# Performance work log

Hardware: AMD Instinct MI355X
Metric: run time of the kernel (lower is better)

The kernel has to match this reference:

```python
import jax, jax.numpy as jnp
import numpy as np

NUM_NODES = 100000
EMBED_DIM = 128
NUM_RELATIONS = 64
BATCH = 512


def setup_inputs() -> dict:
    key = jax.random.key(0)
    k1, k2, k3, k4, k5 = jax.random.split(key, 5)
    u = jax.random.randint(k1, (BATCH,), 0, NUM_NODES)
    v = jax.random.randint(k2, (BATCH,), 0, NUM_NODES)
    r = jax.random.randint(k3, (BATCH,), 0, NUM_RELATIONS)
    node_embeddings = jax.random.normal(k4, (NUM_NODES, EMBED_DIM), dtype=jnp.float32)
    relation_matrices = jax.random.normal(k5, (NUM_RELATIONS, EMBED_DIM, EMBED_DIM), dtype=jnp.float32)
    return {"u": u, "v": v, "r": r,
            "node_embeddings": node_embeddings,
            "relation_matrices": relation_matrices}


def reference(u, v, r, node_embeddings, relation_matrices):
    u_embed = node_embeddings[u]            # [B, D]
    v_embed = node_embeddings[v]            # [B, D]
    rel = relation_matrices[r]              # [B, D, D] per-sample gathered matrices
    # torch.matmul([B,D], [B,D,D]) broadcasts u_embed over the relation batch -> [B_rel, B_u, D]
    score = jnp.einsum('ud,bde->bue', u_embed, rel)   # [B, B, D]
    # matmul with v_embed.T [D, B] -> [B, B, B]
    score = jnp.einsum('bue,ve->buv', score, v_embed)  # [B, B, B]
    return jax.nn.sigmoid(score)
```

## Files before the change

kernel.cpp:

```cpp
#include <hip/hip_runtime.h>


#define BATCH 512
#define DIM   128
#define NRELS 64
#define NTHR  256

typedef float floatx4 __attribute__((ext_vector_type(4)));

__global__ __launch_bounds__(NTHR, 4)
void rad_phaseA_kernel(const int* __restrict__ u_idx,
                       const float* __restrict__ nodes,
                       const float* __restrict__ rels,
                       float* __restrict__ T_ws)
{
    const int rel = (int)blockIdx.x >> 3;
    const int ut0 = ((int)blockIdx.x & 7) * 64;

    __shared__ __align__(16) float UEsT[DIM * 64];
    __shared__ __align__(16) float Rs[16 * DIM];

    const int t  = (int)threadIdx.x;
    const int tu = t >> 4;
    const int tx = t & 15;

    for (int i = t; i < 64 * (DIM / 4); i += NTHR) {
        const int row = i & 63;
        const int dc  = i >> 6;
        const float4 val = *reinterpret_cast<const float4*>(
            nodes + (size_t)u_idx[ut0 + row] * DIM + dc * 4);
        UEsT[(dc * 4 + 0) * 64 + row] = val.x;
        UEsT[(dc * 4 + 1) * 64 + row] = val.y;
        UEsT[(dc * 4 + 2) * 64 + row] = val.z;
        UEsT[(dc * 4 + 3) * 64 + row] = val.w;
    }

    float accA[4][8];
    #pragma unroll
    for (int i = 0; i < 4; ++i)
        #pragma unroll
        for (int j = 0; j < 8; ++j) accA[i][j] = 0.f;

    const float* Rbase = rels + (size_t)rel * DIM * DIM;
    for (int dch = 0; dch < DIM / 16; ++dch) {
        __syncthreads();
        for (int i = t; i < 16 * (DIM / 4); i += NTHR) {
            const int rr = i >> 5;
            const int cc = i & 31;
            *reinterpret_cast<float4*>(Rs + rr * DIM + cc * 4) =
                *reinterpret_cast<const float4*>(
                    Rbase + (size_t)(dch * 16 + rr) * DIM + cc * 4);
        }
        __syncthreads();
        #pragma unroll
        for (int dd = 0; dd < 16; ++dd) {
            const int d = dch * 16 + dd;
            const float4 a  = *reinterpret_cast<const float4*>(UEsT + d * 64 + tu * 4);
            const float4 b0 = *reinterpret_cast<const float4*>(Rs + dd * DIM + tx * 4);
            const float4 b1 = *reinterpret_cast<const float4*>(Rs + dd * DIM + 64 + tx * 4);
            const float av[4] = {a.x, a.y, a.z, a.w};
            const float bv[8] = {b0.x, b0.y, b0.z, b0.w, b1.x, b1.y, b1.z, b1.w};
            #pragma unroll
            for (int i = 0; i < 4; ++i)
                #pragma unroll
                for (int j = 0; j < 8; ++j)
                    accA[i][j] = fmaf(av[i], bv[j], accA[i][j]);
        }
    }

    #pragma unroll
    for (int i = 0; i < 4; ++i) {
        float* rowp = T_ws + ((size_t)rel * BATCH + ut0 + tu * 4 + i) * DIM;
        *reinterpret_cast<float4*>(rowp + tx * 4) =
            make_float4(accA[i][0], accA[i][1], accA[i][2], accA[i][3]);
        *reinterpret_cast<float4*>(rowp + 64 + tx * 4) =
            make_float4(accA[i][4], accA[i][5], accA[i][6], accA[i][7]);
    }
}

__global__ __launch_bounds__(NTHR, 2)
void rad_phaseB_kernel(const int* __restrict__ v_idx,
                       const int* __restrict__ r_idx,
                       const float* __restrict__ nodes,
                       const float* __restrict__ T_ws,
                       float* __restrict__ out)
{
    const int bid = (int)blockIdx.x;
    const int rel = bid >> 6;
    const int ut0 = ((bid >> 3) & 7) * 64;
    const int vt0 = (bid & 7) * 64;

    __shared__ int s_match[BATCH];
    __shared__ int s_mc;
    __shared__ __align__(16) float TsT[DIM * 64];
    __shared__ __align__(16) float VEsT[DIM * 64];

    const int t  = (int)threadIdx.x;
    const int tu = t >> 4;
    const int tx = t & 15;

    if (t == 0) s_mc = 0;
    __syncthreads();
    for (int i = t; i < BATCH; i += NTHR) {
        if (r_idx[i] == rel) {
            int p = atomicAdd(&s_mc, 1);
            s_match[p] = i;
        }
    }
    __syncthreads();
    const int mc = s_mc;
    if (mc == 0) return;

    for (int i = t; i < 64 * (DIM / 4); i += NTHR) {
        const int row = i & 63;
        const int ec  = i >> 6;
        const float4 val = *reinterpret_cast<const float4*>(
            T_ws + ((size_t)rel * BATCH + ut0 + row) * DIM + ec * 4);
        TsT[(ec * 4 + 0) * 64 + row] = val.x;
        TsT[(ec * 4 + 1) * 64 + row] = val.y;
        TsT[(ec * 4 + 2) * 64 + row] = val.z;
        TsT[(ec * 4 + 3) * 64 + row] = val.w;
    }
    for (int i = t; i < 64 * (DIM / 4); i += NTHR) {
        const int row = i & 63;
        const int ec  = i >> 6;
        const float4 val = *reinterpret_cast<const float4*>(
            nodes + (size_t)v_idx[vt0 + row] * DIM + ec * 4);
        VEsT[(ec * 4 + 0) * 64 + row] = val.x;
        VEsT[(ec * 4 + 1) * 64 + row] = val.y;
        VEsT[(ec * 4 + 2) * 64 + row] = val.z;
        VEsT[(ec * 4 + 3) * 64 + row] = val.w;
    }
    __syncthreads();

    float acc[4][4];
    #pragma unroll
    for (int i = 0; i < 4; ++i)
        #pragma unroll
        for (int j = 0; j < 4; ++j) acc[i][j] = 0.f;

    #pragma unroll 8
    for (int e = 0; e < DIM; ++e) {
        const float4 a = *reinterpret_cast<const float4*>(TsT  + e * 64 + tu * 4);
        const float4 b = *reinterpret_cast<const float4*>(VEsT + e * 64 + tx * 4);
        const float av[4] = {a.x, a.y, a.z, a.w};
        const float bv[4] = {b.x, b.y, b.z, b.w};
        #pragma unroll
        for (int i = 0; i < 4; ++i)
            #pragma unroll
            for (int j = 0; j < 4; ++j)
                acc[i][j] = fmaf(av[i], bv[j], acc[i][j]);
    }

    floatx4 sg[4];
    #pragma unroll
    for (int i = 0; i < 4; ++i) {
        sg[i].x = 1.f / (1.f + __expf(-acc[i][0]));
        sg[i].y = 1.f / (1.f + __expf(-acc[i][1]));
        sg[i].z = 1.f / (1.f + __expf(-acc[i][2]));
        sg[i].w = 1.f / (1.f + __expf(-acc[i][3]));
    }

    for (int m = 0; m < mc; ++m) {
        const int bb = s_match[m];
        float* obase = out + (size_t)bb * BATCH * BATCH;
        #pragma unroll
        for (int i = 0; i < 4; ++i) {
            floatx4* dst = reinterpret_cast<floatx4*>(
                obase + (size_t)(ut0 + tu * 4 + i) * BATCH + vt0 + tx * 4);
            __builtin_nontemporal_store(sg[i], dst);
        }
    }
}

__global__ __launch_bounds__(NTHR, 2)
void rad_fused_kernel(const int* __restrict__ u_idx,
                      const int* __restrict__ v_idx,
                      const int* __restrict__ r_idx,
                      const float* __restrict__ nodes,
                      const float* __restrict__ rels,
                      float* __restrict__ out)
{
    const int rel = (int)blockIdx.x >> 3;
    const int ut0 = ((int)blockIdx.x & 7) * 64;

    __shared__ int s_match[BATCH];
    __shared__ int s_mc;
    __shared__ __align__(16) float s_TsT[DIM * 64];
    __shared__ __align__(16) float s_buf[DIM * 64 + 16 * DIM];

    const int t  = (int)threadIdx.x;
    const int tu = t >> 4;
    const int tx = t & 15;

    if (t == 0) s_mc = 0;
    __syncthreads();
    for (int i = t; i < BATCH; i += NTHR) {
        if (r_idx[i] == rel) {
            int p = atomicAdd(&s_mc, 1);
            s_match[p] = i;
        }
    }

    float* UEsT = s_buf;
    float* Rs   = s_buf + DIM * 64;

    for (int i = t; i < 64 * (DIM / 4); i += NTHR) {
        const int row = i & 63;
        const int dc  = i >> 6;
        const float4 val = *reinterpret_cast<const float4*>(
            nodes + (size_t)u_idx[ut0 + row] * DIM + dc * 4);
        UEsT[(dc * 4 + 0) * 64 + row] = val.x;
        UEsT[(dc * 4 + 1) * 64 + row] = val.y;
        UEsT[(dc * 4 + 2) * 64 + row] = val.z;
        UEsT[(dc * 4 + 3) * 64 + row] = val.w;
    }
    __syncthreads();
    const int mc = s_mc;
    if (mc == 0) return;

    float accA[4][8];
    #pragma unroll
    for (int i = 0; i < 4; ++i)
        #pragma unroll
        for (int j = 0; j < 8; ++j) accA[i][j] = 0.f;

    const float* Rbase = rels + (size_t)rel * DIM * DIM;
    for (int dch = 0; dch < DIM / 16; ++dch) {
        for (int i = t; i < 16 * (DIM / 4); i += NTHR) {
            const int rr = i >> 5;
            const int cc = i & 31;
            *reinterpret_cast<float4*>(Rs + rr * DIM + cc * 4) =
                *reinterpret_cast<const float4*>(
                    Rbase + (size_t)(dch * 16 + rr) * DIM + cc * 4);
        }
        __syncthreads();
        #pragma unroll
        for (int dd = 0; dd < 16; ++dd) {
            const int d = dch * 16 + dd;
            const float4 a  = *reinterpret_cast<const float4*>(UEsT + d * 64 + tu * 4);
            const float4 b0 = *reinterpret_cast<const float4*>(Rs + dd * DIM + tx * 4);
            const float4 b1 = *reinterpret_cast<const float4*>(Rs + dd * DIM + 64 + tx * 4);
            const float av[4] = {a.x, a.y, a.z, a.w};
            const float bv[8] = {b0.x, b0.y, b0.z, b0.w, b1.x, b1.y, b1.z, b1.w};
            #pragma unroll
            for (int i = 0; i < 4; ++i)
                #pragma unroll
                for (int j = 0; j < 8; ++j)
                    accA[i][j] = fmaf(av[i], bv[j], accA[i][j]);
        }
        __syncthreads();
    }

    #pragma unroll
    for (int j = 0; j < 8; ++j) {
        const int e = (j < 4) ? (tx * 4 + j) : (64 + tx * 4 + (j - 4));
        #pragma unroll
        for (int i = 0; i < 4; ++i)
            s_TsT[e * 64 + tu * 4 + i] = accA[i][j];
    }

    float* VEsT = s_buf;
    for (int vt = 0; vt < BATCH / 64; ++vt) {
        __syncthreads();
        for (int i = t; i < 64 * (DIM / 4); i += NTHR) {
            const int row = i & 63;
            const int ec  = i >> 6;
            const float4 val = *reinterpret_cast<const float4*>(
                nodes + (size_t)v_idx[vt * 64 + row] * DIM + ec * 4);
            VEsT[(ec * 4 + 0) * 64 + row] = val.x;
            VEsT[(ec * 4 + 1) * 64 + row] = val.y;
            VEsT[(ec * 4 + 2) * 64 + row] = val.z;
            VEsT[(ec * 4 + 3) * 64 + row] = val.w;
        }
        __syncthreads();

        float acc[4][4];
        #pragma unroll
        for (int i = 0; i < 4; ++i)
            #pragma unroll
            for (int j = 0; j < 4; ++j) acc[i][j] = 0.f;

        #pragma unroll 8
        for (int e = 0; e < DIM; ++e) {
            const float4 a = *reinterpret_cast<const float4*>(s_TsT + e * 64 + tu * 4);
            const float4 b = *reinterpret_cast<const float4*>(VEsT  + e * 64 + tx * 4);
            const float av[4] = {a.x, a.y, a.z, a.w};
            const float bv[4] = {b.x, b.y, b.z, b.w};
            #pragma unroll
            for (int i = 0; i < 4; ++i)
                #pragma unroll
                for (int j = 0; j < 4; ++j)
                    acc[i][j] = fmaf(av[i], bv[j], acc[i][j]);
        }

        floatx4 sg[4];
        #pragma unroll
        for (int i = 0; i < 4; ++i) {
            sg[i].x = 1.f / (1.f + __expf(-acc[i][0]));
            sg[i].y = 1.f / (1.f + __expf(-acc[i][1]));
            sg[i].z = 1.f / (1.f + __expf(-acc[i][2]));
            sg[i].w = 1.f / (1.f + __expf(-acc[i][3]));
        }

        for (int m = 0; m < mc; ++m) {
            const int bb = s_match[m];
            float* obase = out + (size_t)bb * BATCH * BATCH;
            #pragma unroll
            for (int i = 0; i < 4; ++i) {
                floatx4* dst = reinterpret_cast<floatx4*>(
                    obase + (size_t)(ut0 + tu * 4 + i) * BATCH + vt * 64 + tx * 4);
                __builtin_nontemporal_store(sg[i], dst);
            }
        }
    }
}

extern "C" void kernel_launch(void* const* d_in, const int* in_sizes, int n_in,
                              void* d_out, int out_size, void* d_ws, size_t ws_size,
                              hipStream_t stream) {
    const int*   u_idx = (const int*)d_in[0];
    const int*   v_idx = (const int*)d_in[1];
    const int*   r_idx = (const int*)d_in[2];
    const float* nodes = (const float*)d_in[3];
    const float* rels  = (const float*)d_in[4];
    float* out = (float*)d_out;

    const size_t t_bytes = (size_t)NRELS * BATCH * DIM * sizeof(float);
    if (ws_size >= t_bytes) {
        float* T_ws = (float*)d_ws;
        rad_phaseA_kernel<<<dim3(NRELS * 8), dim3(NTHR), 0, stream>>>(
            u_idx, nodes, rels, T_ws);
        rad_phaseB_kernel<<<dim3(NRELS * 8 * 8), dim3(NTHR), 0, stream>>>(
            v_idx, r_idx, nodes, T_ws, out);
    } else {
        rad_fused_kernel<<<dim3(NRELS * 8), dim3(NTHR), 0, stream>>>(
            u_idx, v_idx, r_idx, nodes, rels, out);
    }
}
```

Before: 157.3 us.

## Materialize per-relation score planes then broadcast-copy into output

Replaces the two-phase scheme, which wrote a T workspace and then did per-tile scattered stores to every matching batch row, with a new pipeline. The first kernel computes the full sigmoid score plane S for each of the 64 relations in a single fused kernel. The second kernel is a plain streaming copy from S[r[b]] into out[b]. The aim is to make the 512 MB output write a uniform, load-balanced stream and avoid the uneven per-block work in the old phase B. In exchange it adds a 64 MB intermediate write and a full read of S during the copy, and it needs a larger workspace or else it falls back to the fused kernel.

```diff
diff --git a/kernel.cpp b/kernel.cpp
--- a/kernel.cpp
+++ b/kernel.cpp
@@ -8,21 +8,25 @@
 
 typedef float floatx4 __attribute__((ext_vector_type(4)));
 
-__global__ __launch_bounds__(NTHR, 4)
-void rad_phaseA_kernel(const int* __restrict__ u_idx,
-                       const float* __restrict__ nodes,
-                       const float* __restrict__ rels,
-                       float* __restrict__ T_ws)
+__global__ __launch_bounds__(NTHR, 2)
+void rad_computeS_kernel(const int* __restrict__ u_idx,
+                         const int* __restrict__ v_idx,
+                         const float* __restrict__ nodes,
+                         const float* __restrict__ rels,
+                         float* __restrict__ S)
 {
     const int rel = (int)blockIdx.x >> 3;
     const int ut0 = ((int)blockIdx.x & 7) * 64;
 
-    __shared__ __align__(16) float UEsT[DIM * 64];
-    __shared__ __align__(16) float Rs[16 * DIM];
+    __shared__ __align__(16) float s_TsT[DIM * 64];
+    __shared__ __align__(16) float s_buf[DIM * 64 + 16 * DIM];
 
     const int t  = (int)threadIdx.x;
     const int tu = t >> 4;
     const int tx = t & 15;
+
+    float* UEsT = s_buf;
+    float* Rs   = s_buf + DIM * 64;
 
     for (int i = t; i < 64 * (DIM / 4); i += NTHR) {
         const int row = i & 63;
@@ -34,6 +38,7 @@
         UEsT[(dc * 4 + 2) * 64 + row] = val.z;
         UEsT[(dc * 4 + 3) * 64 + row] = val.w;
     }
+    __syncthreads();
 
     float accA[4][8];
     #pragma unroll
@@ -43,7 +48,6 @@
 
     const float* Rbase = rels + (size_t)rel * DIM * DIM;
     for (int dch = 0; dch < DIM / 16; ++dch) {
-        __syncthreads();
         for (int i = t; i < 16 * (DIM / 4); i += NTHR) {
             const int rr = i >> 5;
             const int cc = i & 31;
@@ -66,110 +70,84 @@
                 for (int j = 0; j < 8; ++j)
                     accA[i][j] = fmaf(av[i], bv[j], accA[i][j]);
         }
+        __syncthreads();
     }
 
     #pragma unroll
-    for (int i = 0; i < 4; ++i) {
-        float* rowp = T_ws + ((size_t)rel * BATCH + ut0 + tu * 4 + i) * DIM;
-        *reinterpret_cast<float4*>(rowp + tx * 4) =
-            make_float4(accA[i][0], accA[i][1], accA[i][2], accA[i][3]);
-        *reinterpret_cast<float4*>(rowp + 64 + tx * 4) =
-            make_float4(accA[i][4], accA[i][5], accA[i][6], accA[i][7]);
+    for (int j = 0; j < 8; ++j) {
+        const int e = (j < 4) ? (tx * 4 + j) : (64 + tx * 4 + (j - 4));
+        #pragma unroll
+        for (int i = 0; i < 4; ++i)
+            s_TsT[e * 64 + tu * 4 + i] = accA[i][j];
+    }
+
+    float* VEsT = s_buf;
+    float* Splane = S + (size_t)rel * BATCH * BATCH;
+    for (int vt = 0; vt < BATCH / 64; ++vt) {
+        __syncthreads();
+        for (int i = t; i < 64 * (DIM / 4); i += NTHR) {
+            const int row = i & 63;
+            const int ec  = i >> 6;
+            const float4 val = *reinterpret_cast<const float4*>(
+                nodes + (size_t)v_idx[vt * 64 + row] * DIM + ec * 4);
+            VEsT[(ec * 4 + 0) * 64 + row] = val.x;
+            VEsT[(ec * 4 + 1) * 64 + row] = val.y;
+            VEsT[(ec * 4 + 2) * 64 + row] = val.z;
+            VEsT[(ec * 4 + 3) * 64 + row] = val.w;
+        }
+        __syncthreads();
+
+        float acc[4][4];
+        #pragma unroll
+        for (int i = 0; i < 4; ++i)
+            #pragma unroll
+            for (int j = 0; j < 4; ++j) acc[i][j] = 0.f;
+
+        #pragma unroll 8
+        for (int e = 0; e < DIM; ++e) {
+            const float4 a = *reinterpret_cast<const float4*>(s_TsT + e * 64 + tu * 4);
+            const float4 b = *reinterpret_cast<const float4*>(VEsT  + e * 64 + tx * 4);
+            const float av[4] = {a.x, a.y, a.z, a.w};
+            const float bv[4] = {b.x, b.y, b.z, b.w};
+            #pragma unroll
+            for (int i = 0; i < 4; ++i)
+                #pragma unroll
+                for (int j = 0; j < 4; ++j)
+                    acc[i][j] = fmaf(av[i], bv[j], acc[i][j]);
+        }
+
+        #pragma unroll
+        for (int i = 0; i < 4; ++i) {
+            float4 sg;
+            sg.x = 1.f / (1.f + __expf(-acc[i][0]));
+            sg.y = 1.f / (1.f + __expf(-acc[i][1]));
+            sg.z = 1.f / (1.f + __expf(-acc[i][2]));
+            sg.w = 1.f / (1.f + __expf(-acc[i][3]));
+            *reinterpret_cast<float4*>(
+                Splane + (size_t)(ut0 + tu * 4 + i) * BATCH + vt * 64 + tx * 4) = sg;
+        }
     }
 }
 
-__global__ __launch_bounds__(NTHR, 2)
-void rad_phaseB_kernel(const int* __restrict__ v_idx,
-                       const int* __restrict__ r_idx,
-                       const float* __restrict__ nodes,
-                       const float* __restrict__ T_ws,
-                       float* __restrict__ out)
+__global__ __launch_bounds__(NTHR)
+void rad_copy_kernel(const int* __restrict__ r_idx,
+                     const float* __restrict__ S,
+                     float* __restrict__ out)
 {
-    const int bid = (int)blockIdx.x;
-    const int rel = bid >> 6;
-    const int ut0 = ((bid >> 3) & 7) * 64;
-    const int vt0 = (bid & 7) * 64;
-
-    __shared__ int s_match[BATCH];
-    __shared__ int s_mc;
-    __shared__ __align__(16) float TsT[DIM * 64];
-    __shared__ __align__(16) float VEsT[DIM * 64];
-
-    const int t  = (int)threadIdx.x;
-    const int tu = t >> 4;
-    const int tx = t & 15;
-
-    if (t == 0) s_mc = 0;
-    __syncthreads();
-    for (int i = t; i < BATCH; i += NTHR) {
-        if (r_idx[i] == rel) {
-            int p = atomicAdd(&s_mc, 1);
-            s_match[p] = i;
-        }
-    }
-    __syncthreads();
-    const int mc = s_mc;
-    if (mc == 0) return;
-
-    for (int i = t; i < 64 * (DIM / 4); i += NTHR) {
-        const int row = i & 63;
-        const int ec  = i >> 6;
-        const float4 val = *reinterpret_cast<const float4*>(
-            T_ws + ((size_t)rel * BATCH + ut0 + row) * DIM + ec * 4);
-        TsT[(ec * 4 + 0) * 64 + row] = val.x;
-        TsT[(ec * 4 + 1) * 64 + row] = val.y;
-        TsT[(ec * 4 + 2) * 64 + row] = val.z;
-        TsT[(ec * 4 + 3) * 64 + row] = val.w;
-    }
-    for (int i = t; i < 64 * (DIM / 4); i += NTHR) {
-        const int row = i & 63;
-        const int ec  = i >> 6;
-        const float4 val = *reinterpret_cast<const float4*>(
-            nodes + (size_t)v_idx[vt0 + row] * DIM + ec * 4);
-        VEsT[(ec * 4 + 0) * 64 + row] = val.x;
-        VEsT[(ec * 4 + 1) * 64 + row] = val.y;
-        VEsT[(ec * 4 + 2) * 64 + row] = val.z;
-        VEsT[(ec * 4 + 3) * 64 + row] = val.w;
-    }
-    __syncthreads();
-
-    float acc[4][4];
-    #pragma unroll
-    for (int i = 0; i < 4; ++i)
-        #pragma unroll
-        for (int j = 0; j < 4; ++j) acc[i][j] = 0.f;
-
-    #pragma unroll 8
-    for (int e = 0; e < DIM; ++e) {
-        const float4 a = *reinterpret_cast<const float4*>(TsT  + e * 64 + tu * 4);
-        const float4 b = *reinterpret_cast<const float4*>(VEsT + e * 64 + tx * 4);
-        const float av[4] = {a.x, a.y, a.z, a.w};
-        const float bv[4] = {b.x, b.y, b.z, b.w};
-        #pragma unroll
-        for (int i = 0; i < 4; ++i)
-            #pragma unroll
-            for (int j = 0; j < 4; ++j)
-                acc[i][j] = fmaf(av[i], bv[j], acc[i][j]);
-    }
-
-    floatx4 sg[4];
-    #pragma unroll
-    for (int i = 0; i < 4; ++i) {
-        sg[i].x = 1.f / (1.f + __expf(-acc[i][0]));
-        sg[i].y = 1.f / (1.f + __expf(-acc[i][1]));
-        sg[i].z = 1.f / (1.f + __expf(-acc[i][2]));
-        sg[i].w = 1.f / (1.f + __expf(-acc[i][3]));
-    }
-
-    for (int m = 0; m < mc; ++m) {
-        const int bb = s_match[m];
-        float* obase = out + (size_t)bb * BATCH * BATCH;
-        #pragma unroll
-        for (int i = 0; i < 4; ++i) {
-            floatx4* dst = reinterpret_cast<floatx4*>(
-                obase + (size_t)(ut0 + tu * 4 + i) * BATCH + vt0 + tx * 4);
-            __builtin_nontemporal_store(sg[i], dst);
-        }
+    const int bid   = (int)blockIdx.x;
+    const int b     = bid >> 3;
+    const int slice = bid & 7;
+    const int rel   = r_idx[b];
+
+    const float* src = S   + ((size_t)rel * BATCH + slice * 64) * BATCH;
+    float*       dst = out + ((size_t)b   * BATCH + slice * 64) * BATCH;
+
+    const int t = (int)threadIdx.x;
+    #pragma unroll 4
+    for (int i = t; i < 64 * BATCH / 4; i += NTHR) {
+        const floatx4 v = *reinterpret_cast<const floatx4*>(src + i * 4);
+        __builtin_nontemporal_store(
+            v, reinterpret_cast<floatx4*>(dst + i * 4));
     }
 }
 
@@ -326,13 +304,13 @@
     const float* rels  = (const float*)d_in[4];
     float* out = (float*)d_out;
 
-    const size_t t_bytes = (size_t)NRELS * BATCH * DIM * sizeof(float);
-    if (ws_size >= t_bytes) {
-        float* T_ws = (float*)d_ws;
-        rad_phaseA_kernel<<<dim3(NRELS * 8), dim3(NTHR), 0, stream>>>(
-            u_idx, nodes, rels, T_ws);
-        rad_phaseB_kernel<<<dim3(NRELS * 8 * 8), dim3(NTHR), 0, stream>>>(
-            v_idx, r_idx, nodes, T_ws, out);
+    const size_t s_bytes = (size_t)NRELS * BATCH * BATCH * sizeof(float);
+    if (ws_size >= s_bytes) {
+        float* S = (float*)d_ws;
+        rad_computeS_kernel<<<dim3(NRELS * 8), dim3(NTHR), 0, stream>>>(
+            u_idx, v_idx, nodes, rels, S);
+        rad_copy_kernel<<<dim3(BATCH * 8), dim3(NTHR), 0, stream>>>(
+            r_idx, S, out);
     } else {
         rad_fused_kernel<<<dim3(NRELS * 8), dim3(NTHR), 0, stream>>>(
             u_idx, v_idx, r_idx, nodes, rels, out);
```

New measurement: 216.6 us. +37.7%, slower.

## Precompute relation match lists and store T transposed for direct tile loads

Applied to the files above, without the earlier changes.

An extra block in the phase-A kernel now builds per-relation lists of the batch indices that use each relation, and phase A writes T in a [rel][e][u] transposed layout. Phase B no longer scans r_idx with shared-memory atomics in every block and can load its T tile with plain float4 copies instead of scattered transposing stores to shared memory. The cost is a larger workspace requirement, and the two-kernel path is skipped when the workspace is too small.

```diff
diff --git a/kernel.cpp b/kernel.cpp
--- a/kernel.cpp
+++ b/kernel.cpp
@@ -8,19 +8,43 @@
 
 typedef float floatx4 __attribute__((ext_vector_type(4)));
 
-__global__ __launch_bounds__(NTHR, 4)
-void rad_phaseA_kernel(const int* __restrict__ u_idx,
-                       const float* __restrict__ nodes,
-                       const float* __restrict__ rels,
-                       float* __restrict__ T_ws)
+#define T_ELEMS   ((size_t)NRELS * DIM * BATCH)
+#define CNT_OFF   (T_ELEMS)
+#define LIST_OFF  (T_ELEMS + 64)
+#define WS_NEED   ((T_ELEMS + 64 + (size_t)NRELS * BATCH) * 4)
+
+__global__ __launch_bounds__(NTHR, 2)
+void rad_prep_kernel(const int* __restrict__ u_idx,
+                     const int* __restrict__ r_idx,
+                     const float* __restrict__ nodes,
+                     const float* __restrict__ rels,
+                     float* __restrict__ ws)
 {
-    const int rel = (int)blockIdx.x >> 3;
-    const int ut0 = ((int)blockIdx.x & 7) * 64;
+    const int bid = (int)blockIdx.x;
+    const int t   = (int)threadIdx.x;
+
+    if (bid == NRELS * 8) {
+        __shared__ int s_cnt[NRELS];
+        int* counts = (int*)(ws + CNT_OFF);
+        int* lists  = (int*)(ws + LIST_OFF);
+        if (t < NRELS) s_cnt[t] = 0;
+        __syncthreads();
+        for (int i = t; i < BATCH; i += NTHR) {
+            const int rel = r_idx[i];
+            const int pos = atomicAdd(&s_cnt[rel], 1);
+            lists[rel * BATCH + pos] = i;
+        }
+        __syncthreads();
+        if (t < NRELS) counts[t] = s_cnt[t];
+        return;
+    }
+
+    const int rel = bid >> 3;
+    const int ut0 = (bid & 7) * 64;
 
     __shared__ __align__(16) float UEsT[DIM * 64];
     __shared__ __align__(16) float Rs[16 * DIM];
 
-    const int t  = (int)threadIdx.x;
     const int tu = t >> 4;
     const int tx = t & 15;
 
@@ -69,29 +93,30 @@
     }
 
     #pragma unroll
-    for (int i = 0; i < 4; ++i) {
-        float* rowp = T_ws + ((size_t)rel * BATCH + ut0 + tu * 4 + i) * DIM;
-        *reinterpret_cast<float4*>(rowp + tx * 4) =
-            make_float4(accA[i][0], accA[i][1], accA[i][2], accA[i][3]);
-        *reinterpret_cast<float4*>(rowp + 64 + tx * 4) =
-            make_float4(accA[i][4], accA[i][5], accA[i][6], accA[i][7]);
+    for (int j = 0; j < 8; ++j) {
+        const int e = (j < 4) ? (tx * 4 + j) : (64 + tx * 4 + (j - 4));
+        float4 w4 = make_float4(accA[0][j], accA[1][j], accA[2][j], accA[3][j]);
+        *reinterpret_cast<float4*>(
+            ws + ((size_t)rel * DIM + e) * BATCH + ut0 + tu * 4) = w4;
     }
 }
 
 __global__ __launch_bounds__(NTHR, 2)
-void rad_phaseB_kernel(const int* __restrict__ v_idx,
-                       const int* __restrict__ r_idx,
-                       const float* __restrict__ nodes,
-                       const float* __restrict__ T_ws,
-                       float* __restrict__ out)
+void rad_tile_kernel(const int* __restrict__ v_idx,
+                     const float* __restrict__ nodes,
+                     const float* __restrict__ ws,
+                     float* __restrict__ out)
 {
     const int bid = (int)blockIdx.x;
     const int rel = bid >> 6;
     const int ut0 = ((bid >> 3) & 7) * 64;
     const int vt0 = (bid & 7) * 64;
 
-    __shared__ int s_match[BATCH];
-    __shared__ int s_mc;
+    const int* counts = (const int*)(ws + CNT_OFF);
+    const int* lists  = (const int*)(ws + LIST_OFF) + rel * BATCH;
+    const int  mc     = counts[rel];
+    if (mc == 0) return;
+
     __shared__ __align__(16) float TsT[DIM * 64];
     __shared__ __align__(16) float VEsT[DIM * 64];
 
@@ -99,27 +124,12 @@
     const int tu = t >> 4;
     const int tx = t & 15;
 
-    if (t == 0) s_mc = 0;
-    __syncthreads();
-    for (int i = t; i < BATCH; i += NTHR) {
-        if (r_idx[i] == rel) {
-            int p = atomicAdd(&s_mc, 1);
-            s_match[p] = i;
-        }
-    }
-    __syncthreads();
-    const int mc = s_mc;
-    if (mc == 0) return;
-
-    for (int i = t; i < 64 * (DIM / 4); i += NTHR) {
-        const int row = i & 63;
-        const int ec  = i >> 6;
-        const float4 val = *reinterpret_cast<const float4*>(
-            T_ws + ((size_t)rel * BATCH + ut0 + row) * DIM + ec * 4);
-        TsT[(ec * 4 + 0) * 64 + row] = val.x;
-        TsT[(ec * 4 + 1) * 64 + row] = val.y;
-        TsT[(ec * 4 + 2) * 64 + row] = val.z;
-        TsT[(ec * 4 + 3) * 64 + row] = val.w;
+    const float* Tbase = ws + (size_t)rel * DIM * BATCH + ut0;
+    for (int i = t; i < DIM * 16; i += NTHR) {
+        const int e  = i >> 4;
+        const int uc = i & 15;
+        *reinterpret_cast<float4*>(TsT + e * 64 + uc * 4) =
+            *reinterpret_cast<const float4*>(Tbase + (size_t)e * BATCH + uc * 4);
     }
     for (int i = t; i < 64 * (DIM / 4); i += NTHR) {
         const int row = i & 63;
@@ -162,13 +172,13 @@
     }
 
     for (int m = 0; m < mc; ++m) {
-        const int bb = s_match[m];
-        float* obase = out + (size_t)bb * BATCH * BATCH;
+        const int bb = lists[m];
+        float* obase = out + (size_t)bb * BATCH * BATCH + vt0 + tx * 4;
         #pragma unroll
         for (int i = 0; i < 4; ++i) {
-            floatx4* dst = reinterpret_cast<floatx4*>(
-                obase + (size_t)(ut0 + tu * 4 + i) * BATCH + vt0 + tx * 4);
-            __builtin_nontemporal_store(sg[i], dst);
+            __builtin_nontemporal_store(
+                sg[i], reinterpret_cast<floatx4*>(
+                           obase + (size_t)(ut0 + tu * 4 + i) * BATCH));
         }
     }
 }
@@ -326,13 +336,12 @@
     const float* rels  = (const float*)d_in[4];
     float* out = (float*)d_out;
 
-    const size_t t_bytes = (size_t)NRELS * BATCH * DIM * sizeof(float);
-    if (ws_size >= t_bytes) {
-        float* T_ws = (float*)d_ws;
-        rad_phaseA_kernel<<<dim3(NRELS * 8), dim3(NTHR), 0, stream>>>(
-            u_idx, nodes, rels, T_ws);
-        rad_phaseB_kernel<<<dim3(NRELS * 8 * 8), dim3(NTHR), 0, stream>>>(
-            v_idx, r_idx, nodes, T_ws, out);
+    if (ws_size >= WS_NEED) {
+        float* ws = (float*)d_ws;
+        rad_prep_kernel<<<dim3(NRELS * 8 + 1), dim3(NTHR), 0, stream>>>(
+            u_idx, r_idx, nodes, rels, ws);
+        rad_tile_kernel<<<dim3(NRELS * 8 * 8), dim3(NTHR), 0, stream>>>(
+            v_idx, nodes, ws, out);
     } else {
         rad_fused_kernel<<<dim3(NRELS * 8), dim3(NTHR), 0, stream>>>(
             u_idx, v_idx, r_idx, nodes, rels, out);
```

Result: no change. 154.7 us (-1.6%).
